# Kernel tuning notes

Hardware: AMD Instinct MI355X
Metric: run time of the kernel (lower is better)

The kernel has to match this reference:

```python
import jax, jax.numpy as jnp
import numpy as np

B, T, D = 4, 4096, 1024
LN_EPS = 1e-5

def _xavier(key, shape, gain=1.0):
    fan_in, fan_out = shape[1], shape[0]
    a = gain * np.sqrt(6.0 / (fan_in + fan_out))
    return jax.random.uniform(key, shape, jnp.float32, -a, a)

def setup_inputs() -> dict:
    key = jax.random.key(0)
    kx, kg, kv, ko = jax.random.split(key, 4)
    # log_decay param init so that softplus(log_decay) == decay_init (0.01)
    log_decay = jnp.asarray(np.log(np.expm1(0.01)), jnp.float32)
    return {
        "x": jax.random.normal(kx, (B, T, D), jnp.float32),
        "ln_w": jnp.ones((D,), jnp.float32),
        "ln_b": jnp.zeros((D,), jnp.float32),
        "gate_w": _xavier(kg, (D, D)),            # torch Linear weight [out, in]
        "gate_b": jnp.zeros((D,), jnp.float32),
        "value_w": _xavier(kv, (D, D), gain=0.01),
        "value_b": jnp.zeros((D,), jnp.float32),
        "out_w": _xavier(ko, (D, D), gain=0.01),
        "out_b": jnp.zeros((D,), jnp.float32),
        "log_decay": log_decay,
    }

def reference(x, ln_w, ln_b, gate_w, gate_b, value_w, value_b, out_w, out_b, log_decay):
    # LayerNorm over last dim
    mu = jnp.mean(x, axis=-1, keepdims=True)
    var = jnp.mean(jnp.square(x - mu), axis=-1, keepdims=True)
    normed = (x - mu) * jax.lax.rsqrt(var + LN_EPS) * ln_w + ln_b
    # gate / value projections (torch Linear: y = x @ W.T + b)
    g = jax.nn.sigmoid(normed @ gate_w.T + gate_b)
    v = normed @ value_w.T + value_b
    # push-pull: cumsum(g*v) - cumsum((1-g)*v) == cumsum((2g-1)*v)
    cumsum = jnp.cumsum((2.0 * g - 1.0) * v, axis=1)
    alpha = jax.nn.softplus(log_decay)
    positions = jnp.arange(T, dtype=jnp.float32)
    decay = jnp.exp(-alpha * positions)[None, :, None]  # [1, T, 1]
    output = cumsum * decay
    return x + (output @ out_w.T + out_b)
```

## Files before the change

### kernel.cpp

```cpp
#include <hip/hip_runtime.h>
#include <hip/hip_bf16.h>

#define BB 4
#define TT 4096
#define DD 1024
#define MM (BB * TT)
#define LN_EPS 1e-5f

#define NC 64
#define CL 64

typedef __attribute__((ext_vector_type(8))) short bf16x8;
typedef __attribute__((ext_vector_type(4))) float f32x4;

__device__ __forceinline__ float bfbits2f(unsigned short h) {
    return __uint_as_float(((unsigned int)h) << 16);
}
__device__ __forceinline__ unsigned short f2bfbits(float f) {
    __hip_bfloat16 h = __float2bfloat16(f);
    return *reinterpret_cast<unsigned short*>(&h);
}
__device__ __forceinline__ unsigned int pack2(float a, float b) {
    return (unsigned int)f2bfbits(a) | ((unsigned int)f2bfbits(b) << 16);
}

__device__ __forceinline__ void async_copy16(void* lds, const void* g) {
    __builtin_amdgcn_global_load_lds(
        (const __attribute__((address_space(1))) void*)g,
        (__attribute__((address_space(3))) void*)lds,
        16, 0, 0);
}

__global__ __launch_bounds__(256)
void prep_kernel(const float* __restrict__ s0, const float* __restrict__ s1,
                 const float* __restrict__ s2,
                 __hip_bfloat16* __restrict__ d0, __hip_bfloat16* __restrict__ d1,
                 __hip_bfloat16* __restrict__ d2,
                 const float* __restrict__ x,
                 const float* __restrict__ lnw,
                 const float* __restrict__ lnb,
                 __hip_bfloat16* __restrict__ normed)
{
    if (blockIdx.x < 3072) {
        const int blk = blockIdx.x;
        const int w = blk >> 10;
        const float* src = (w == 0) ? s0 : (w == 1) ? s1 : s2;
        __hip_bfloat16* dst = (w == 0) ? d0 : (w == 1) ? d1 : d2;
        const size_t i = ((size_t)(blk & 1023) * 256 + threadIdx.x) * 4;
        float4 v = *(const float4*)(src + i);
        uint2 o;
        o.x = pack2(v.x, v.y);
        o.y = pack2(v.z, v.w);
        *(uint2*)((unsigned short*)dst + i) = o;
        return;
    }
    const int wv   = threadIdx.x >> 6;
    const int lane = threadIdx.x & 63;
    const int row  = (blockIdx.x - 3072) * 4 + wv;

    const float* xr = x + (size_t)row * DD + lane * 16;
    float4 v[4];
    #pragma unroll
    for (int i = 0; i < 4; ++i) v[i] = *(const float4*)(xr + i * 4);

    float s = 0.0f, ss = 0.0f;
    #pragma unroll
    for (int i = 0; i < 4; ++i) {
        s  += (v[i].x + v[i].y) + (v[i].z + v[i].w);
        ss += fmaf(v[i].x, v[i].x, fmaf(v[i].y, v[i].y,
              fmaf(v[i].z, v[i].z, v[i].w * v[i].w)));
    }
    #pragma unroll
    for (int o = 32; o > 0; o >>= 1) {
        s  += __shfl_down(s, o);
        ss += __shfl_down(ss, o);
    }
    s  = __shfl(s, 0);
    ss = __shfl(ss, 0);

    const float mu   = s * (1.0f / DD);
    const float var  = ss * (1.0f / DD) - mu * mu;
    const float rstd = rsqrtf(var + LN_EPS);

    unsigned int res[8];
    #pragma unroll
    for (int i = 0; i < 4; ++i) {
        float4 wr = *(const float4*)(lnw + lane * 16 + i * 4);
        float4 br = *(const float4*)(lnb + lane * 16 + i * 4);
        float o0 = (v[i].x - mu) * rstd * wr.x + br.x;
        float o1 = (v[i].y - mu) * rstd * wr.y + br.y;
        float o2 = (v[i].z - mu) * rstd * wr.z + br.z;
        float o3 = (v[i].w - mu) * rstd * wr.w + br.w;
        res[i * 2]     = pack2(o0, o1);
        res[i * 2 + 1] = pack2(o2, o3);
    }
    unsigned short* op = (unsigned short*)normed + (size_t)row * DD + lane * 16;
    *(uint4*)op       = make_uint4(res[0], res[1], res[2], res[3]);
    *(uint4*)(op + 8) = make_uint4(res[4], res[5], res[6], res[7]);
}

__global__ __launch_bounds__(256, 2)
void dual_gemm_gate(const __hip_bfloat16* __restrict__ A,
                    const __hip_bfloat16* __restrict__ Wg,
                    const __hip_bfloat16* __restrict__ Wv,
                    const float* __restrict__ gb,
                    const float* __restrict__ vb,
                    __hip_bfloat16* __restrict__ U,
                    float* __restrict__ Pk,
                    int M, int N, int K)
{
    constexpr int BK = 64;
    __shared__ short As[128 * BK];
    __shared__ short Bg[128 * BK];
    __shared__ short Bv[128 * BK];

    const int tid  = threadIdx.x;
    const int m0   = blockIdx.x * 128;
    const int n0   = blockIdx.y * 128;
    const int wave = tid >> 6;
    const int lane = tid & 63;
    const int wm   = (wave & 1) * 64;
    const int wn   = (wave >> 1) * 64;
    const int lrow = lane & 15;
    const int kgrp = lane >> 4;
    const int swz  = lrow & 7;

    f32x4 accg[4][4] = {};
    f32x4 accv[4][4] = {};

    const __hip_bfloat16* gA[4];
    const __hip_bfloat16* gG[4];
    const __hip_bfloat16* gV[4];
    #pragma unroll
    for (int r = 0; r < 4; ++r) {
        const int slot = r * 256 + tid;
        const int srow = slot >> 3;
        const int gcc  = (slot & 7) ^ (srow & 7);
        gA[r] = A  + (size_t)(m0 + srow) * K + gcc * 8;
        gG[r] = Wg + (size_t)(n0 + srow) * K + gcc * 8;
        gV[r] = Wv + (size_t)(n0 + srow) * K + gcc * 8;
    }

    for (int k0 = 0; k0 < K; k0 += BK) {
        #pragma unroll
        for (int r = 0; r < 4; ++r) {
            async_copy16(&As[(r * 256 + tid) * 8], gA[r] + k0);
            async_copy16(&Bg[(r * 256 + tid) * 8], gG[r] + k0);
            async_copy16(&Bv[(r * 256 + tid) * 8], gV[r] + k0);
        }
        __builtin_amdgcn_s_waitcnt(0);
        __syncthreads();

        #pragma unroll
        for (int ks = 0; ks < 2; ++ks) {
            const int co = ((ks * 4 + kgrp) ^ swz) * 8;
            bf16x8 af[4], bgf[4], bvf[4];
            #pragma unroll
            for (int i = 0; i < 4; ++i)
                af[i] = *(const bf16x8*)&As[(wm + i * 16 + lrow) * BK + co];
            #pragma unroll
            for (int j = 0; j < 4; ++j) {
                bgf[j] = *(const bf16x8*)&Bg[(wn + j * 16 + lrow) * BK + co];
                bvf[j] = *(const bf16x8*)&Bv[(wn + j * 16 + lrow) * BK + co];
            }
            #pragma unroll
            for (int i = 0; i < 4; ++i)
                #pragma unroll
                for (int j = 0; j < 4; ++j) {
                    accg[i][j] = __builtin_amdgcn_mfma_f32_16x16x32_bf16(
                        bgf[j], af[i], accg[i][j], 0, 0, 0);
                    accv[i][j] = __builtin_amdgcn_mfma_f32_16x16x32_bf16(
                        bvf[j], af[i], accv[i][j], 0, 0, 0);
                }
        }
        __syncthreads();
    }

    const int chrow = m0 + wm;
    const int cb    = chrow >> 12;
    const int cc    = (chrow & (TT - 1)) >> 6;

    #pragma unroll
    for (int j = 0; j < 4; ++j) {
        const int nb = n0 + wn + j * 16 + kgrp * 4;
        const float4 gb4 = *(const float4*)(gb + nb);
        const float4 vb4 = *(const float4*)(vb + nb);
        float4 ps = make_float4(0.f, 0.f, 0.f, 0.f);
        #pragma unroll
        for (int i = 0; i < 4; ++i) {
            const int m = m0 + wm + i * 16 + lrow;
            const float g0 = accg[i][j][0] + gb4.x, v0 = accv[i][j][0] + vb4.x;
            const float g1 = accg[i][j][1] + gb4.y, v1 = accv[i][j][1] + vb4.y;
            const float g2 = accg[i][j][2] + gb4.z, v2 = accv[i][j][2] + vb4.z;
            const float g3 = accg[i][j][3] + gb4.w, v3 = accv[i][j][3] + vb4.w;
            const float u0 = (2.0f / (1.0f + __expf(-g0)) - 1.0f) * v0;
            const float u1 = (2.0f / (1.0f + __expf(-g1)) - 1.0f) * v1;
            const float u2 = (2.0f / (1.0f + __expf(-g2)) - 1.0f) * v2;
            const float u3 = (2.0f / (1.0f + __expf(-g3)) - 1.0f) * v3;
            ps.x += u0; ps.y += u1; ps.z += u2; ps.w += u3;
            uint2 o;
            o.x = pack2(u0, u1);
            o.y = pack2(u2, u3);
            *(uint2*)((unsigned short*)U + (size_t)m * N + nb) = o;
        }
        #pragma unroll
        for (int mk = 1; mk <= 8; mk <<= 1) {
            ps.x += __shfl_xor(ps.x, mk);
            ps.y += __shfl_xor(ps.y, mk);
            ps.z += __shfl_xor(ps.z, mk);
            ps.w += __shfl_xor(ps.w, mk);
        }
        if (lrow == 0)
            *(float4*)&Pk[((size_t)cb * NC + cc) * DD + nb] = ps;
    }
}

__global__ __launch_bounds__(256, 2)
void gemm_out(const __hip_bfloat16* __restrict__ A,
              const __hip_bfloat16* __restrict__ W,
              const float* __restrict__ bias,
              const float* __restrict__ X,
              float* __restrict__ C,
              int M, int N, int K)
{
    constexpr int BK = 64;
    __shared__ short As[128 * BK];
    __shared__ short Bs[128 * BK];

    const int tid  = threadIdx.x;
    const int m0   = blockIdx.x * 128;
    const int n0   = blockIdx.y * 128;
    const int wave = tid >> 6;
    const int lane = tid & 63;
    const int wm   = (wave & 1) * 64;
    const int wn   = (wave >> 1) * 64;
    const int lrow = lane & 15;
    const int kgrp = lane >> 4;
    const int swz  = lrow & 7;

    f32x4 acc[4][4] = {};

    const __hip_bfloat16* gA[4];
    const __hip_bfloat16* gB[4];
    #pragma unroll
    for (int r = 0; r < 4; ++r) {
        const int slot = r * 256 + tid;
        const int srow = slot >> 3;
        const int gcc  = (slot & 7) ^ (srow & 7);
        gA[r] = A + (size_t)(m0 + srow) * K + gcc * 8;
        gB[r] = W + (size_t)(n0 + srow) * K + gcc * 8;
    }

    for (int k0 = 0; k0 < K; k0 += BK) {
        #pragma unroll
        for (int r = 0; r < 4; ++r) {
            async_copy16(&As[(r * 256 + tid) * 8], gA[r] + k0);
            async_copy16(&Bs[(r * 256 + tid) * 8], gB[r] + k0);
        }
        __builtin_amdgcn_s_waitcnt(0);
        __syncthreads();

        #pragma unroll
        for (int ks = 0; ks < 2; ++ks) {
            const int co = ((ks * 4 + kgrp) ^ swz) * 8;
            bf16x8 af[4], bfr[4];
            #pragma unroll
            for (int i = 0; i < 4; ++i)
                af[i] = *(const bf16x8*)&As[(wm + i * 16 + lrow) * BK + co];
            #pragma unroll
            for (int j = 0; j < 4; ++j)
                bfr[j] = *(const bf16x8*)&Bs[(wn + j * 16 + lrow) * BK + co];
            #pragma unroll
            for (int i = 0; i < 4; ++i)
                #pragma unroll
                for (int j = 0; j < 4; ++j)
                    acc[i][j] = __builtin_amdgcn_mfma_f32_16x16x32_bf16(
                        bfr[j], af[i], acc[i][j], 0, 0, 0);
        }
        __syncthreads();
    }

    #pragma unroll
    for (int j = 0; j < 4; ++j) {
        const int nb = n0 + wn + j * 16 + kgrp * 4;
        const float4 bv = *(const float4*)(bias + nb);
        #pragma unroll
        for (int i = 0; i < 4; ++i) {
            const int m = m0 + wm + i * 16 + lrow;
            const size_t idx = (size_t)m * N + nb;
            const float4 xv = *(const float4*)(X + idx);
            float4 o;
            o.x = acc[i][j][0] + bv.x + xv.x;
            o.y = acc[i][j][1] + bv.y + xv.y;
            o.z = acc[i][j][2] + bv.z + xv.z;
            o.w = acc[i][j][3] + bv.w + xv.w;
            *(float4*)(C + idx) = o;
        }
    }
}

__global__ __launch_bounds__(1024)
void scan_final(const __hip_bfloat16* __restrict__ U,
                const float* __restrict__ Pk,
                const float* __restrict__ log_decay,
                __hip_bfloat16* __restrict__ S)
{
    __shared__ float LdsC[8][DD];
    __shared__ float LdsP[8][DD];

    const int c  = blockIdx.x, b = blockIdx.y;
    const int w  = threadIdx.x >> 7;
    const int dg = threadIdx.x & 127;
    const int d8 = dg * 8;

    const float ld    = log_decay[0];
    const float alpha = log1pf(__expf(ld));
    const float ratio = __expf(-alpha);

    const size_t base = ((size_t)b * TT + (size_t)c * CL + w * 8) * DD + d8;
    const unsigned short* up = (const unsigned short*)U + base;

    uint4 raw[8];
    float cs[8] = {0.f, 0.f, 0.f, 0.f, 0.f, 0.f, 0.f, 0.f};
    #pragma unroll
    for (int r = 0; r < 8; ++r) {
        raw[r] = *(const uint4*)(up + (size_t)r * DD);
        const unsigned int wds[4] = {raw[r].x, raw[r].y, raw[r].z, raw[r].w};
        #pragma unroll
        for (int k = 0; k < 4; ++k) {
            cs[2 * k]     += bfbits2f((unsigned short)(wds[k] & 0xFFFF));
            cs[2 * k + 1] += bfbits2f((unsigned short)(wds[k] >> 16));
        }
    }

    float pp[8] = {0.f, 0.f, 0.f, 0.f, 0.f, 0.f, 0.f, 0.f};
    for (int cc = w; cc < c; cc += 8) {
        const float* pr = &Pk[((size_t)b * NC + cc) * DD + d8];
        const float4 a0 = *(const float4*)pr;
        const float4 a1 = *(const float4*)(pr + 4);
        pp[0] += a0.x; pp[1] += a0.y; pp[2] += a0.z; pp[3] += a0.w;
        pp[4] += a1.x; pp[5] += a1.y; pp[6] += a1.z; pp[7] += a1.w;
    }

    *(float4*)&LdsC[w][d8]     = make_float4(cs[0], cs[1], cs[2], cs[3]);
    *(float4*)&LdsC[w][d8 + 4] = make_float4(cs[4], cs[5], cs[6], cs[7]);
    *(float4*)&LdsP[w][d8]     = make_float4(pp[0], pp[1], pp[2], pp[3]);
    *(float4*)&LdsP[w][d8 + 4] = make_float4(pp[4], pp[5], pp[6], pp[7]);
    __syncthreads();

    float run[8] = {0.f, 0.f, 0.f, 0.f, 0.f, 0.f, 0.f, 0.f};
    #pragma unroll
    for (int w2 = 0; w2 < 8; ++w2) {
        const float4 p0 = *(const float4*)&LdsP[w2][d8];
        const float4 p1 = *(const float4*)&LdsP[w2][d8 + 4];
        run[0] += p0.x; run[1] += p0.y; run[2] += p0.z; run[3] += p0.w;
        run[4] += p1.x; run[5] += p1.y; run[6] += p1.z; run[7] += p1.w;
        if (w2 < w) {
            const float4 c0 = *(const float4*)&LdsC[w2][d8];
            const float4 c1 = *(const float4*)&LdsC[w2][d8 + 4];
            run[0] += c0.x; run[1] += c0.y; run[2] += c0.z; run[3] += c0.w;
            run[4] += c1.x; run[5] += c1.y; run[6] += c1.z; run[7] += c1.w;
        }
    }

    float dec = __expf(-alpha * (float)(c * CL + w * 8));
    unsigned short* sp = (unsigned short*)S + base;
    #pragma unroll
    for (int r = 0; r < 8; ++r) {
        const unsigned int wds[4] = {raw[r].x, raw[r].y, raw[r].z, raw[r].w};
        uint4 o;
        unsigned int* ow = (unsigned int*)&o;
        #pragma unroll
        for (int k = 0; k < 4; ++k) {
            run[2 * k]     += bfbits2f((unsigned short)(wds[k] & 0xFFFF));
            run[2 * k + 1] += bfbits2f((unsigned short)(wds[k] >> 16));
            ow[k] = pack2(run[2 * k] * dec, run[2 * k + 1] * dec);
        }
        *(uint4*)(sp + (size_t)r * DD) = o;
        dec *= ratio;
    }
}

extern "C" void kernel_launch(void* const* d_in, const int* in_sizes, int n_in,
                              void* d_out, int out_size, void* d_ws, size_t ws_size,
                              hipStream_t stream)
{
    const float* x        = (const float*)d_in[0];
    const float* ln_w     = (const float*)d_in[1];
    const float* ln_b     = (const float*)d_in[2];
    const float* gate_w   = (const float*)d_in[3];
    const float* gate_b   = (const float*)d_in[4];
    const float* value_w  = (const float*)d_in[5];
    const float* value_b  = (const float*)d_in[6];
    const float* out_w    = (const float*)d_in[7];
    const float* out_b    = (const float*)d_in[8];
    const float* log_dec  = (const float*)d_in[9];
    float* out = (float*)d_out;

    char* ws = (char*)d_ws;
    const size_t MB = 1024 * 1024;
    __hip_bfloat16* normed = (__hip_bfloat16*)(ws);
    __hip_bfloat16* S      = (__hip_bfloat16*)(ws);
    float*          Pk     = (float*)(ws + 32 * MB);
    __hip_bfloat16* Wg16   = (__hip_bfloat16*)(ws + 33 * MB);
    __hip_bfloat16* Wv16   = (__hip_bfloat16*)(ws + 35 * MB);
    __hip_bfloat16* Wo16   = (__hip_bfloat16*)(ws + 37 * MB);
    __hip_bfloat16* U      = (__hip_bfloat16*)d_out;

    prep_kernel<<<dim3(3072 + MM / 4), dim3(256), 0, stream>>>(
        gate_w, value_w, out_w, Wg16, Wv16, Wo16, x, ln_w, ln_b, normed);

    dual_gemm_gate<<<dim3(MM / 128, DD / 128), dim3(256), 0, stream>>>(
        normed, Wg16, Wv16, gate_b, value_b, U, Pk, MM, DD, DD);

    scan_final<<<dim3(NC, BB), dim3(1024), 0, stream>>>(U, Pk, log_dec, S);

    gemm_out<<<dim3(MM / 128, DD / 128), dim3(256), 0, stream>>>(
        S, Wo16, out_b, x, out, MM, DD, DD);
}
```

Baseline: 282.4 us.

## Interleave gate/value weights and use 256x256 double-buffered pipelined GEMM tiles

Gate and value weights are interleaved row-wise into one 2048-row bf16 matrix, so the dual GEMM runs as a single 2048-wide GEMM whose accumulator pairs hold (g, v) for adjacent outputs. Both GEMMs now use a shared 256x256 tile main loop with 512 threads, double-buffered LDS, async global-to-LDS prefetch with partial vmcnt waits, raw barriers and s_setprio around MFMA clusters. The goal is to overlap loads with MFMA work and raise arithmetic intensity per block. In exchange it uses more LDS and registers per block, and the manual waitcnt and barrier ordering is fragile.

```diff
diff --git a/kernel.cpp b/kernel.cpp
--- a/kernel.cpp
+++ b/kernel.cpp
@@ -31,11 +31,13 @@
         16, 0, 0);
 }
 
+#define RAW_BAR() asm volatile("s_barrier" ::: "memory")
+
 __global__ __launch_bounds__(256)
 void prep_kernel(const float* __restrict__ s0, const float* __restrict__ s1,
                  const float* __restrict__ s2,
-                 __hip_bfloat16* __restrict__ d0, __hip_bfloat16* __restrict__ d1,
-                 __hip_bfloat16* __restrict__ d2,
+                 __hip_bfloat16* __restrict__ dGV,
+                 __hip_bfloat16* __restrict__ dO,
                  const float* __restrict__ x,
                  const float* __restrict__ lnw,
                  const float* __restrict__ lnb,
@@ -45,13 +47,16 @@
         const int blk = blockIdx.x;
         const int w = blk >> 10;
         const float* src = (w == 0) ? s0 : (w == 1) ? s1 : s2;
-        __hip_bfloat16* dst = (w == 0) ? d0 : (w == 1) ? d1 : d2;
         const size_t i = ((size_t)(blk & 1023) * 256 + threadIdx.x) * 4;
         float4 v = *(const float4*)(src + i);
         uint2 o;
         o.x = pack2(v.x, v.y);
         o.y = pack2(v.z, v.w);
-        *(uint2*)((unsigned short*)dst + i) = o;
+        size_t di;
+        if (w == 2) di = i;
+        else        di = ((((i >> 10) << 1) | (size_t)w) << 10) | (i & 1023);
+        __hip_bfloat16* dst = (w == 2) ? dO : dGV;
+        *(uint2*)((unsigned short*)dst + di) = o;
         return;
     }
     const int wv   = threadIdx.x >> 6;
@@ -99,201 +104,341 @@
     *(uint4*)(op + 8) = make_uint4(res[4], res[5], res[6], res[7]);
 }
 
-__global__ __launch_bounds__(256, 2)
+__device__ __forceinline__ void kloop256(
+    const __hip_bfloat16* __restrict__ Aglb,
+    const __hip_bfloat16* __restrict__ Bglb,
+    short* Ab0, short* Ab1, short* Bb0, short* Bb1,
+    int m0, int n0, int tid, f32x4 acc[8][4])
+{
+    constexpr int BK = 64;
+    constexpr int K  = DD;
+    const int lane = tid & 63;
+    const int wave = tid >> 6;
+    const int wrow = (wave & 1) * 128;
+    const int wcol = (wave >> 1) * 64;
+    const int lrow = lane & 15;
+    const int kgrp = lane >> 4;
+    const int swz  = lrow & 7;
+
+    const __hip_bfloat16* gA[4];
+    const __hip_bfloat16* gB[4];
+    #pragma unroll
+    for (int r = 0; r < 4; ++r) {
+        const int slot = r * 512 + tid;
+        const int srow = slot >> 3;
+        const int gcc  = (slot & 7) ^ (srow & 7);
+        gA[r] = Aglb + (size_t)(m0 + srow) * K + gcc * 8;
+        gB[r] = Bglb + (size_t)(n0 + srow) * K + gcc * 8;
+    }
+    auto stA = [&](short* buf, int kofs) {
+        #pragma unroll
+        for (int r = 0; r < 4; ++r)
+            async_copy16(&buf[(r * 512 + tid) * 8], gA[r] + kofs);
+    };
+    auto stB = [&](short* buf, int kofs) {
+        #pragma unroll
+        for (int r = 0; r < 4; ++r)
+            async_copy16(&buf[(r * 512 + tid) * 8], gB[r] + kofs);
+    };
+
+    stA(Ab0, 0);
+    stB(Bb0, 0);
+    stA(Ab1, BK);
+    asm volatile("s_waitcnt vmcnt(4)" ::: "memory");
+    __builtin_amdgcn_s_barrier();
+
+    bf16x8 a[4][2], b01[2][2], b23[2][2];
+
+    for (int it = 0; it < 8; ++it) {
+        const bool sT2 = (2 * it + 2) < 16;
+        const bool sT3 = (2 * it + 3) < 16;
+        const int kB1 = (2 * it + 1) * BK;
+        const int kT2 = (2 * it + 2) * BK;
+        const int kT3 = (2 * it + 3) * BK;
+
+        #pragma unroll
+        for (int f = 0; f < 4; ++f)
+            #pragma unroll
+            for (int ks = 0; ks < 2; ++ks)
+                a[f][ks] = *(const bf16x8*)&Ab0[(wrow + f * 16 + lrow) * BK +
+                                                (((ks * 4 + kgrp) ^ swz) * 8)];
+        #pragma unroll
+        for (int j = 0; j < 2; ++j)
+            #pragma unroll
+            for (int ks = 0; ks < 2; ++ks)
+                b01[j][ks] = *(const bf16x8*)&Bb0[(wcol + j * 16 + lrow) * BK +
+                                                  (((ks * 4 + kgrp) ^ swz) * 8)];
+        stB(Bb1, kB1);
+        RAW_BAR();
+        __builtin_amdgcn_s_setprio(1);
+        #pragma unroll
+        for (int ks = 0; ks < 2; ++ks)
+            #pragma unroll
+            for (int f = 0; f < 4; ++f)
+                #pragma unroll
+                for (int j = 0; j < 2; ++j)
+                    acc[f][j] = __builtin_amdgcn_mfma_f32_16x16x32_bf16(
+                        b01[j][ks], a[f][ks], acc[f][j], 0, 0, 0);
+        __builtin_amdgcn_s_setprio(0);
+        RAW_BAR();
+
+        #pragma unroll
+        for (int j = 0; j < 2; ++j)
+            #pragma unroll
+            for (int ks = 0; ks < 2; ++ks)
+                b23[j][ks] = *(const bf16x8*)&Bb0[(wcol + 32 + j * 16 + lrow) * BK +
+                                                  (((ks * 4 + kgrp) ^ swz) * 8)];
+        RAW_BAR();
+        __builtin_amdgcn_s_setprio(1);
+        #pragma unroll
+        for (int ks = 0; ks < 2; ++ks)
+            #pragma unroll
+            for (int f = 0; f < 4; ++f)
+                #pragma unroll
+                for (int j = 0; j < 2; ++j)
+                    acc[f][2 + j] = __builtin_amdgcn_mfma_f32_16x16x32_bf16(
+                        b23[j][ks], a[f][ks], acc[f][2 + j], 0, 0, 0);
+        __builtin_amdgcn_s_setprio(0);
+        RAW_BAR();
+
+        #pragma unroll
+        for (int f = 0; f < 4; ++f)
+            #pragma unroll
+            for (int ks = 0; ks < 2; ++ks)
+                a[f][ks] = *(const bf16x8*)&Ab0[(wrow + 64 + f * 16 + lrow) * BK +
+                                                (((ks * 4 + kgrp) ^ swz) * 8)];
+        RAW_BAR();
+        __builtin_amdgcn_s_setprio(1);
+        #pragma unroll
+        for (int ks = 0; ks < 2; ++ks)
+            #pragma unroll
+            for (int f = 0; f < 4; ++f)
+                #pragma unroll
+                for (int j = 0; j < 2; ++j)
+                    acc[4 + f][j] = __builtin_amdgcn_mfma_f32_16x16x32_bf16(
+                        b01[j][ks], a[f][ks], acc[4 + f][j], 0, 0, 0);
+        __builtin_amdgcn_s_setprio(0);
+        RAW_BAR();
+
+        if (sT2) stA(Ab0, kT2);
+        if (sT2) asm volatile("s_waitcnt vmcnt(4)" ::: "memory");
+        else     asm volatile("s_waitcnt vmcnt(0)" ::: "memory");
+        RAW_BAR();
+        __builtin_amdgcn_s_setprio(1);
+        #pragma unroll
+        for (int ks = 0; ks < 2; ++ks)
+            #pragma unroll
+            for (int f = 0; f < 4; ++f)
+                #pragma unroll
+                for (int j = 0; j < 2; ++j)
+                    acc[4 + f][2 + j] = __builtin_amdgcn_mfma_f32_16x16x32_bf16(
+                        b23[j][ks], a[f][ks], acc[4 + f][2 + j], 0, 0, 0);
+        __builtin_amdgcn_s_setprio(0);
+        RAW_BAR();
+
+        #pragma unroll
+        for (int f = 0; f < 4; ++f)
+            #pragma unroll
+            for (int ks = 0; ks < 2; ++ks)
+                a[f][ks] = *(const bf16x8*)&Ab1[(wrow + f * 16 + lrow) * BK +
+                                                (((ks * 4 + kgrp) ^ swz) * 8)];
+        #pragma unroll
+        for (int j = 0; j < 2; ++j)
+            #pragma unroll
+            for (int ks = 0; ks < 2; ++ks)
+                b01[j][ks] = *(const bf16x8*)&Bb1[(wcol + j * 16 + lrow) * BK +
+                                                  (((ks * 4 + kgrp) ^ swz) * 8)];
+        if (sT2) stB(Bb0, kT2);
+        RAW_BAR();
+        __builtin_amdgcn_s_setprio(1);
+        #pragma unroll
+        for (int ks = 0; ks < 2; ++ks)
+            #pragma unroll
+            for (int f = 0; f < 4; ++f)
+                #pragma unroll
+                for (int j = 0; j < 2; ++j)
+                    acc[f][j] = __builtin_amdgcn_mfma_f32_16x16x32_bf16(
+                        b01[j][ks], a[f][ks], acc[f][j], 0, 0, 0);
+        __builtin_amdgcn_s_setprio(0);
+        RAW_BAR();
+
+        #pragma unroll
+        for (int j = 0; j < 2; ++j)
+            #pragma unroll
+            for (int ks = 0; ks < 2; ++ks)
+                b23[j][ks] = *(const bf16x8*)&Bb1[(wcol + 32 + j * 16 + lrow) * BK +
+                                                  (((ks * 4 + kgrp) ^ swz) * 8)];
+        RAW_BAR();
+        __builtin_amdgcn_s_setprio(1);
+        #pragma unroll
+        for (int ks = 0; ks < 2; ++ks)
+            #pragma unroll
+            for (int f = 0; f < 4; ++f)
+                #pragma unroll
+                for (int j = 0; j < 2; ++j)
+                    acc[f][2 + j] = __builtin_amdgcn_mfma_f32_16x16x32_bf16(
+                        b23[j][ks], a[f][ks], acc[f][2 + j], 0, 0, 0);
+        __builtin_amdgcn_s_setprio(0);
+        RAW_BAR();
+
+        #pragma unroll
+        for (int f = 0; f < 4; ++f)
+            #pragma unroll
+            for (int ks = 0; ks < 2; ++ks)
+                a[f][ks] = *(const bf16x8*)&Ab1[(wrow + 64 + f * 16 + lrow) * BK +
+                                                (((ks * 4 + kgrp) ^ swz) * 8)];
+        RAW_BAR();
+        __builtin_amdgcn_s_setprio(1);
+        #pragma unroll
+        for (int ks = 0; ks < 2; ++ks)
+            #pragma unroll
+            for (int f = 0; f < 4; ++f)
+                #pragma unroll
+                for (int j = 0; j < 2; ++j)
+                    acc[4 + f][j] = __builtin_amdgcn_mfma_f32_16x16x32_bf16(
+                        b01[j][ks], a[f][ks], acc[4 + f][j], 0, 0, 0);
+        __builtin_amdgcn_s_setprio(0);
+        RAW_BAR();
+
+        if (sT3) stA(Ab1, kT3);
+        if (it < 7) {
+            if (sT3) asm volatile("s_waitcnt vmcnt(4)" ::: "memory");
+            else     asm volatile("s_waitcnt vmcnt(0)" ::: "memory");
+        }
+        RAW_BAR();
+        __builtin_amdgcn_s_setprio(1);
+        #pragma unroll
+        for (int ks = 0; ks < 2; ++ks)
+            #pragma unroll
+            for (int f = 0; f < 4; ++f)
+                #pragma unroll
+                for (int j = 0; j < 2; ++j)
+                    acc[4 + f][2 + j] = __builtin_amdgcn_mfma_f32_16x16x32_bf16(
+                        b23[j][ks], a[f][ks], acc[4 + f][2 + j], 0, 0, 0);
+        __builtin_amdgcn_s_setprio(0);
+        RAW_BAR();
+    }
+}
+
+__global__ __launch_bounds__(512, 2)
 void dual_gemm_gate(const __hip_bfloat16* __restrict__ A,
-                    const __hip_bfloat16* __restrict__ Wg,
-                    const __hip_bfloat16* __restrict__ Wv,
+                    const __hip_bfloat16* __restrict__ Wgv,
                     const float* __restrict__ gb,
                     const float* __restrict__ vb,
                     __hip_bfloat16* __restrict__ U,
-                    float* __restrict__ Pk,
-                    int M, int N, int K)
+                    float* __restrict__ Pk)
 {
-    constexpr int BK = 64;
-    __shared__ short As[128 * BK];
-    __shared__ short Bg[128 * BK];
-    __shared__ short Bv[128 * BK];
-
-    const int tid  = threadIdx.x;
-    const int m0   = blockIdx.x * 128;
-    const int n0   = blockIdx.y * 128;
+    __shared__ short Ab[2][256 * 64];
+    __shared__ short Bb[2][256 * 64];
+
+    const int tid = threadIdx.x;
+    const int m0  = blockIdx.x * 256;
+    const int n0  = blockIdx.y * 256;
+
+    f32x4 acc[8][4] = {};
+    kloop256(A, Wgv, Ab[0], Ab[1], Bb[0], Bb[1], m0, n0, tid, acc);
+
+    const int lane = tid & 63;
     const int wave = tid >> 6;
-    const int lane = tid & 63;
-    const int wm   = (wave & 1) * 64;
-    const int wn   = (wave >> 1) * 64;
+    const int wrow = (wave & 1) * 128;
+    const int wcol = (wave >> 1) * 64;
     const int lrow = lane & 15;
     const int kgrp = lane >> 4;
-    const int swz  = lrow & 7;
-
-    f32x4 accg[4][4] = {};
-    f32x4 accv[4][4] = {};
-
-    const __hip_bfloat16* gA[4];
-    const __hip_bfloat16* gG[4];
-    const __hip_bfloat16* gV[4];
-    #pragma unroll
-    for (int r = 0; r < 4; ++r) {
-        const int slot = r * 256 + tid;
-        const int srow = slot >> 3;
-        const int gcc  = (slot & 7) ^ (srow & 7);
-        gA[r] = A  + (size_t)(m0 + srow) * K + gcc * 8;
-        gG[r] = Wg + (size_t)(n0 + srow) * K + gcc * 8;
-        gV[r] = Wv + (size_t)(n0 + srow) * K + gcc * 8;
-    }
-
-    for (int k0 = 0; k0 < K; k0 += BK) {
-        #pragma unroll
-        for (int r = 0; r < 4; ++r) {
-            async_copy16(&As[(r * 256 + tid) * 8], gA[r] + k0);
-            async_copy16(&Bg[(r * 256 + tid) * 8], gG[r] + k0);
-            async_copy16(&Bv[(r * 256 + tid) * 8], gV[r] + k0);
-        }
-        __builtin_amdgcn_s_waitcnt(0);
-        __syncthreads();
-
-        #pragma unroll
-        for (int ks = 0; ks < 2; ++ks) {
-            const int co = ((ks * 4 + kgrp) ^ swz) * 8;
-            bf16x8 af[4], bgf[4], bvf[4];
-            #pragma unroll
-            for (int i = 0; i < 4; ++i)
-                af[i] = *(const bf16x8*)&As[(wm + i * 16 + lrow) * BK + co];
-            #pragma unroll
-            for (int j = 0; j < 4; ++j) {
-                bgf[j] = *(const bf16x8*)&Bg[(wn + j * 16 + lrow) * BK + co];
-                bvf[j] = *(const bf16x8*)&Bv[(wn + j * 16 + lrow) * BK + co];
-            }
-            #pragma unroll
-            for (int i = 0; i < 4; ++i)
-                #pragma unroll
-                for (int j = 0; j < 4; ++j) {
-                    accg[i][j] = __builtin_amdgcn_mfma_f32_16x16x32_bf16(
-                        bgf[j], af[i], accg[i][j], 0, 0, 0);
-                    accv[i][j] = __builtin_amdgcn_mfma_f32_16x16x32_bf16(
-                        bvf[j], af[i], accv[i][j], 0, 0, 0);
-                }
-        }
-        __syncthreads();
-    }
-
-    const int chrow = m0 + wm;
-    const int cb    = chrow >> 12;
-    const int cc    = (chrow & (TT - 1)) >> 6;
-
+
+    const int dbase = ((n0 + wcol) >> 1) + kgrp * 2;
+    float2 gb2[4], vb2[4];
     #pragma unroll
     for (int j = 0; j < 4; ++j) {
-        const int nb = n0 + wn + j * 16 + kgrp * 4;
-        const float4 gb4 = *(const float4*)(gb + nb);
-        const float4 vb4 = *(const float4*)(vb + nb);
-        float4 ps = make_float4(0.f, 0.f, 0.f, 0.f);
-        #pragma unroll
-        for (int i = 0; i < 4; ++i) {
-            const int m = m0 + wm + i * 16 + lrow;
-            const float g0 = accg[i][j][0] + gb4.x, v0 = accv[i][j][0] + vb4.x;
-            const float g1 = accg[i][j][1] + gb4.y, v1 = accv[i][j][1] + vb4.y;
-            const float g2 = accg[i][j][2] + gb4.z, v2 = accv[i][j][2] + vb4.z;
-            const float g3 = accg[i][j][3] + gb4.w, v3 = accv[i][j][3] + vb4.w;
+        gb2[j] = *(const float2*)(gb + dbase + j * 8);
+        vb2[j] = *(const float2*)(vb + dbase + j * 8);
+    }
+
+    float psx0[4] = {}, psy0[4] = {}, psx1[4] = {}, psy1[4] = {};
+    #pragma unroll
+    for (int f = 0; f < 8; ++f) {
+        const int m = m0 + wrow + f * 16 + lrow;
+        unsigned short* urow = (unsigned short*)U + (size_t)m * DD;
+        #pragma unroll
+        for (int j = 0; j < 4; ++j) {
+            const int db = dbase + j * 8;
+            const float g0 = acc[f][j][0] + gb2[j].x;
+            const float v0 = acc[f][j][1] + vb2[j].x;
+            const float g1 = acc[f][j][2] + gb2[j].y;
+            const float v1 = acc[f][j][3] + vb2[j].y;
             const float u0 = (2.0f / (1.0f + __expf(-g0)) - 1.0f) * v0;
             const float u1 = (2.0f / (1.0f + __expf(-g1)) - 1.0f) * v1;
-            const float u2 = (2.0f / (1.0f + __expf(-g2)) - 1.0f) * v2;
-            const float u3 = (2.0f / (1.0f + __expf(-g3)) - 1.0f) * v3;
-            ps.x += u0; ps.y += u1; ps.z += u2; ps.w += u3;
-            uint2 o;
-            o.x = pack2(u0, u1);
-            o.y = pack2(u2, u3);
-            *(uint2*)((unsigned short*)U + (size_t)m * N + nb) = o;
-        }
+            *(unsigned int*)(urow + db) = pack2(u0, u1);
+            if (f < 4) { psx0[j] += u0; psy0[j] += u1; }
+            else       { psx1[j] += u0; psy1[j] += u1; }
+        }
+    }
+    #pragma unroll
+    for (int j = 0; j < 4; ++j) {
         #pragma unroll
         for (int mk = 1; mk <= 8; mk <<= 1) {
-            ps.x += __shfl_xor(ps.x, mk);
-            ps.y += __shfl_xor(ps.y, mk);
-            ps.z += __shfl_xor(ps.z, mk);
-            ps.w += __shfl_xor(ps.w, mk);
-        }
-        if (lrow == 0)
-            *(float4*)&Pk[((size_t)cb * NC + cc) * DD + nb] = ps;
-    }
-}
-
-__global__ __launch_bounds__(256, 2)
-void gemm_out(const __hip_bfloat16* __restrict__ A,
-              const __hip_bfloat16* __restrict__ W,
+            psx0[j] += __shfl_xor(psx0[j], mk);
+            psy0[j] += __shfl_xor(psy0[j], mk);
+            psx1[j] += __shfl_xor(psx1[j], mk);
+            psy1[j] += __shfl_xor(psy1[j], mk);
+        }
+    }
+    if (lrow == 0) {
+        const int grow = m0 + wrow;
+        const int cb   = grow >> 12;
+        const int cc   = (grow & (TT - 1)) >> 6;
+        #pragma unroll
+        for (int j = 0; j < 4; ++j) {
+            const int db = dbase + j * 8;
+            *(float2*)&Pk[((size_t)cb * NC + cc) * DD + db] =
+                make_float2(psx0[j], psy0[j]);
+            *(float2*)&Pk[((size_t)cb * NC + cc + 1) * DD + db] =
+                make_float2(psx1[j], psy1[j]);
+        }
+    }
+}
+
+__global__ __launch_bounds__(512, 2)
+void gemm_out(const __hip_bfloat16* __restrict__ S,
+              const __hip_bfloat16* __restrict__ Wo,
               const float* __restrict__ bias,
               const float* __restrict__ X,
-              float* __restrict__ C,
-              int M, int N, int K)
+              float* __restrict__ C)
 {
-    constexpr int BK = 64;
-    __shared__ short As[128 * BK];
-    __shared__ short Bs[128 * BK];
-
-    const int tid  = threadIdx.x;
-    const int m0   = blockIdx.x * 128;
-    const int n0   = blockIdx.y * 128;
+    __shared__ short Ab[2][256 * 64];
+    __shared__ short Bb[2][256 * 64];
+
+    const int tid = threadIdx.x;
+    const int m0  = blockIdx.x * 256;
+    const int n0  = blockIdx.y * 256;
+
+    f32x4 acc[8][4] = {};
+    kloop256(S, Wo, Ab[0], Ab[1], Bb[0], Bb[1], m0, n0, tid, acc);
+
+    const int lane = tid & 63;
     const int wave = tid >> 6;
-    const int lane = tid & 63;
-    const int wm   = (wave & 1) * 64;
-    const int wn   = (wave >> 1) * 64;
+    const int wrow = (wave & 1) * 128;
+    const int wcol = (wave >> 1) * 64;
     const int lrow = lane & 15;
     const int kgrp = lane >> 4;
-    const int swz  = lrow & 7;
-
-    f32x4 acc[4][4] = {};
-
-    const __hip_bfloat16* gA[4];
-    const __hip_bfloat16* gB[4];
-    #pragma unroll
-    for (int r = 0; r < 4; ++r) {
-        const int slot = r * 256 + tid;
-        const int srow = slot >> 3;
-        const int gcc  = (slot & 7) ^ (srow & 7);
-        gA[r] = A + (size_t)(m0 + srow) * K + gcc * 8;
-        gB[r] = W + (size_t)(n0 + srow) * K + gcc * 8;
-    }
-
-    for (int k0 = 0; k0 < K; k0 += BK) {
-        #pragma unroll
-        for (int r = 0; r < 4; ++r) {
-            async_copy16(&As[(r * 256 + tid) * 8], gA[r] + k0);
-            async_copy16(&Bs[(r * 256 + tid) * 8], gB[r] + k0);
-        }
-        __builtin_amdgcn_s_waitcnt(0);
-        __syncthreads();
-
-        #pragma unroll
-        for (int ks = 0; ks < 2; ++ks) {
-            const int co = ((ks * 4 + kgrp) ^ swz) * 8;
-            bf16x8 af[4], bfr[4];
-            #pragma unroll
-            for (int i = 0; i < 4; ++i)
-                af[i] = *(const bf16x8*)&As[(wm + i * 16 + lrow) * BK + co];
-            #pragma unroll
-            for (int j = 0; j < 4; ++j)
-                bfr[j] = *(const bf16x8*)&Bs[(wn + j * 16 + lrow) * BK + co];
-            #pragma unroll
-            for (int i = 0; i < 4; ++i)
-                #pragma unroll
-                for (int j = 0; j < 4; ++j)
-                    acc[i][j] = __builtin_amdgcn_mfma_f32_16x16x32_bf16(
-                        bfr[j], af[i], acc[i][j], 0, 0, 0);
-        }
-        __syncthreads();
-    }
-
-    #pragma unroll
-    for (int j = 0; j < 4; ++j) {
-        const int nb = n0 + wn + j * 16 + kgrp * 4;
-        const float4 bv = *(const float4*)(bias + nb);
-        #pragma unroll
-        for (int i = 0; i < 4; ++i) {
-            const int m = m0 + wm + i * 16 + lrow;
-            const size_t idx = (size_t)m * N + nb;
+
+    float4 bv[4];
+    #pragma unroll
+    for (int j = 0; j < 4; ++j)
+        bv[j] = *(const float4*)(bias + n0 + wcol + j * 16 + kgrp * 4);
+
+    #pragma unroll
+    for (int f = 0; f < 8; ++f) {
+        const int m = m0 + wrow + f * 16 + lrow;
+        #pragma unroll
+        for (int j = 0; j < 4; ++j) {
+            const int nb = n0 + wcol + j * 16 + kgrp * 4;
+            const size_t idx = (size_t)m * DD + nb;
             const float4 xv = *(const float4*)(X + idx);
             float4 o;
-            o.x = acc[i][j][0] + bv.x + xv.x;
-            o.y = acc[i][j][1] + bv.y + xv.y;
-            o.z = acc[i][j][2] + bv.z + xv.z;
-            o.w = acc[i][j][3] + bv.w + xv.w;
+            o.x = acc[f][j][0] + bv[j].x + xv.x;
+            o.y = acc[f][j][1] + bv[j].y + xv.y;
+            o.z = acc[f][j][2] + bv[j].z + xv.z;
+            o.w = acc[f][j][3] + bv[j].w + xv.w;
             *(float4*)(C + idx) = o;
         }
     }
@@ -402,19 +547,18 @@
     __hip_bfloat16* normed = (__hip_bfloat16*)(ws);
     __hip_bfloat16* S      = (__hip_bfloat16*)(ws);
     float*          Pk     = (float*)(ws + 32 * MB);
-    __hip_bfloat16* Wg16   = (__hip_bfloat16*)(ws + 33 * MB);
-    __hip_bfloat16* Wv16   = (__hip_bfloat16*)(ws + 35 * MB);
+    __hip_bfloat16* Wgv16  = (__hip_bfloat16*)(ws + 33 * MB);
     __hip_bfloat16* Wo16   = (__hip_bfloat16*)(ws + 37 * MB);
     __hip_bfloat16* U      = (__hip_bfloat16*)d_out;
 
     prep_kernel<<<dim3(3072 + MM / 4), dim3(256), 0, stream>>>(
-        gate_w, value_w, out_w, Wg16, Wv16, Wo16, x, ln_w, ln_b, normed);
-
-    dual_gemm_gate<<<dim3(MM / 128, DD / 128), dim3(256), 0, stream>>>(
-        normed, Wg16, Wv16, gate_b, value_b, U, Pk, MM, DD, DD);
+        gate_w, value_w, out_w, Wgv16, Wo16, x, ln_w, ln_b, normed);
+
+    dual_gemm_gate<<<dim3(MM / 256, 2048 / 256), dim3(512), 0, stream>>>(
+        normed, Wgv16, gate_b, value_b, U, Pk);
 
     scan_final<<<dim3(NC, BB), dim3(1024), 0, stream>>>(U, Pk, log_dec, S);
 
-    gemm_out<<<dim3(MM / 128, DD / 128), dim3(256), 0, stream>>>(
-        S, Wo16, out_b, x, out, MM, DD, DD);
-}
+    gemm_out<<<dim3(MM / 256, DD / 256), dim3(512), 0, stream>>>(
+        S, Wo16, out_b, x, out);
+}
```

After: 266.6 us. 5.6% less time.
